# Kernel optimization log

Measured on AMD Instinct MI355X. Metric: run time of the kernel, lower is better.

The kernel has to match this reference:

```python
import jax, jax.numpy as jnp
import numpy as np

B, T, C, HS = 16, 2048, 2048, 256  # batch, seq (=BLOCK_SIZE), N_EMBD, head_size


def setup_inputs() -> dict:
    key = jax.random.key(0)
    k0, k1, k2, k3 = jax.random.split(key, 4)
    token_embd = jax.random.normal(k0, (B, T, C), dtype=jnp.float32)
    # nn.Linear(C, HS, bias=False); store as [C, HS] so projection is x @ W
    scale = 1.0 / np.sqrt(C)
    Wk = jax.random.normal(k1, (C, HS), dtype=jnp.float32) * scale
    Wq = jax.random.normal(k2, (C, HS), dtype=jnp.float32) * scale
    Wv = jax.random.normal(k3, (C, HS), dtype=jnp.float32) * scale
    return {"token_embd": token_embd, "Wk": Wk, "Wq": Wq, "Wv": Wv}


def reference(token_embd, Wk, Wq, Wv):
    Bc, Tc, Cc = token_embd.shape
    k = token_embd @ Wk  # [B,T,HS]
    q = token_embd @ Wq  # [B,T,HS]
    v = token_embd @ Wv  # [B,T,HS]
    # NOTE faithful quirks of the source: k @ q^T (not q @ k^T) and
    # MULTIPLY by sqrt(C) where C = N_EMBD.
    weights = jnp.einsum("bih,bjh->bij", k, q) * (Cc ** 0.5)  # [B,T,T]
    # causal mask: tril==0 (upper triangle, j>i) -> -inf
    i = jnp.arange(Tc)[:, None]
    j = jnp.arange(Tc)[None, :]
    weights = jnp.where(j > i, -jnp.inf, weights)
    # softmax over dim=1 (rows / first T axis), as in the source
    weights = jax.nn.softmax(weights, axis=1)
    # dropout p=0.0 / eval mode -> identity
    output = jnp.einsum("bij,bjh->bih", weights, v)  # [B,T,HS]
    return output
```

## Files before the change

kernel.cpp:

```cpp
#include <hip/hip_runtime.h>
#include <math.h>

#define Bn 16
#define Tn 2048
#define Cn 2048
#define HSn 256
#define SCALE 45.254833995939045f
#define NEG_BIG (-1e30f)
#define NT 16
#define NPAIR 136
#define WN 524288

typedef __attribute__((ext_vector_type(8))) short bf16x8;
typedef __attribute__((ext_vector_type(4))) float f32x4;
typedef unsigned short u16;
typedef unsigned int u32;

__device__ __forceinline__ u16 bf16_rn(float f) {
    u32 u = __float_as_uint(f);
    u += 0x7fffu + ((u >> 16) & 1u);
    return (u16)(u >> 16);
}
__device__ __forceinline__ float bf16_rn_f(float f) {
    return __uint_as_float((u32)bf16_rn(f) << 16);
}

#define GLOAD_LDS16(gp, lp)                                                      \
    __builtin_amdgcn_global_load_lds(                                            \
        (const __attribute__((address_space(1))) unsigned int*)(gp),             \
        (__attribute__((address_space(3))) unsigned int*)(lp), 16, 0, 0)

__global__ __launch_bounds__(256) void split_w_kernel(
    const float* __restrict__ Wk, const float* __restrict__ Wq,
    const float* __restrict__ Wv, u16* __restrict__ Wt)
{
    const int n = threadIdx.x, k = blockIdx.x, mat = blockIdx.y;
    const float* src = (mat == 0) ? Wk : (mat == 1) ? Wq : Wv;
    const float f = src[(long)k * HSn + n];
    const u32 u = __float_as_uint(f);
    const u16 hb = (u16)(u >> 16);
    const float fh = __uint_as_float(u & 0xffff0000u);
    const u16 lb = bf16_rn(f - fh);
    u16* base = Wt + (long)mat * 2 * WN;
    base[(long)n * Cn + k] = hb;
    base[WN + (long)n * Cn + k] = lb;
}

__global__ __launch_bounds__(256, 2) void projm_fused_kernel(
    const float* __restrict__ X, const u16* __restrict__ Wt,
    u16* __restrict__ Khi, u16* __restrict__ Klo,
    u16* __restrict__ Qhi, u16* __restrict__ Qlo, u16* __restrict__ Vbf)
{
    __shared__ u16 Ahi[2048], Alo[2048];
    __shared__ u16 Bbuf[20480];

    const int tid = threadIdx.x, l = tid & 63, w = tid >> 6;
    const int wm = w & 1, wn = w >> 1;
    const int m0 = blockIdx.x * 64, n0 = blockIdx.y * 128;

    int xoff[2], aoff[2];
    #pragma unroll
    for (int p = 0; p < 2; ++p) {
        const int idx4 = p * 256 + tid;
        const int row  = idx4 >> 3;
        const int kk4  = (idx4 & 7) * 4;
        xoff[p] = (m0 + row) * Cn + kk4;
        aoff[p] = (row >> 4) * 512 + (((row & 15) | ((kk4 >> 3) << 4)) * 8) + (kk4 & 7);
    }

    int wgoff[10];
    const int lbase = w * 10 * 512;
    #pragma unroll
    for (int j = 0; j < 10; ++j) {
        const int g    = w * 10 + j;
        const int half = g >> 3;
        const int cc   = g & 7;
        const int nrow = n0 + cc * 16 + (l & 15);
        wgoff[j] = half * WN + nrow * Cn + ((l >> 4) << 3);
    }

    f32x4 accK[2][4], accQ[2][4], accV[2][4];
    #pragma unroll
    for (int mt = 0; mt < 2; ++mt)
        #pragma unroll
        for (int nt = 0; nt < 4; ++nt)
            #pragma unroll
            for (int r = 0; r < 4; ++r) {
                accK[mt][nt][r] = 0.f; accQ[mt][nt][r] = 0.f; accV[mt][nt][r] = 0.f;
            }

    #pragma unroll 1
    for (int k0 = 0; k0 < Cn; k0 += 32) {
        const float4 xv0 = *(const float4*)(X + xoff[0] + k0);
        const float4 xv1 = *(const float4*)(X + xoff[1] + k0);
        #pragma unroll
        for (int j = 0; j < 10; ++j)
            GLOAD_LDS16(Wt + wgoff[j] + k0, Bbuf + lbase + j * 512);

        #pragma unroll
        for (int p = 0; p < 2; ++p) {
            const float4 xv = p ? xv1 : xv0;
            const float xf[4] = {xv.x, xv.y, xv.z, xv.w};
            ushort4 h4, l4;
            #pragma unroll
            for (int c = 0; c < 4; ++c) {
                const u32 u = __float_as_uint(xf[c]);
                ((u16*)&h4)[c] = (u16)(u >> 16);
                const float fh = __uint_as_float(u & 0xffff0000u);
                ((u16*)&l4)[c] = bf16_rn(xf[c] - fh);
            }
            *(ushort4*)(Ahi + aoff[p]) = h4;
            *(ushort4*)(Alo + aoff[p]) = l4;
        }
        __syncthreads();

        bf16x8 ah[2], al[2];
        #pragma unroll
        for (int mt = 0; mt < 2; ++mt) {
            ah[mt] = *(const bf16x8*)(Ahi + (wm * 2 + mt) * 512 + l * 8);
            al[mt] = *(const bf16x8*)(Alo + (wm * 2 + mt) * 512 + l * 8);
        }
        {
            bf16x8 bh[4], bl[4];
            #pragma unroll
            for (int nt = 0; nt < 4; ++nt) {
                bh[nt] = *(const bf16x8*)(Bbuf + (0 * 8 + wn * 4 + nt) * 512 + l * 8);
                bl[nt] = *(const bf16x8*)(Bbuf + (1 * 8 + wn * 4 + nt) * 512 + l * 8);
            }
            #pragma unroll
            for (int mt = 0; mt < 2; ++mt)
                #pragma unroll
                for (int nt = 0; nt < 4; ++nt) {
                    accK[mt][nt] = __builtin_amdgcn_mfma_f32_16x16x32_bf16(ah[mt], bh[nt], accK[mt][nt], 0, 0, 0);
                    accK[mt][nt] = __builtin_amdgcn_mfma_f32_16x16x32_bf16(ah[mt], bl[nt], accK[mt][nt], 0, 0, 0);
                    accK[mt][nt] = __builtin_amdgcn_mfma_f32_16x16x32_bf16(al[mt], bh[nt], accK[mt][nt], 0, 0, 0);
                }
        }
        {
            bf16x8 bh[4], bl[4];
            #pragma unroll
            for (int nt = 0; nt < 4; ++nt) {
                bh[nt] = *(const bf16x8*)(Bbuf + (2 * 8 + wn * 4 + nt) * 512 + l * 8);
                bl[nt] = *(const bf16x8*)(Bbuf + (3 * 8 + wn * 4 + nt) * 512 + l * 8);
            }
            #pragma unroll
            for (int mt = 0; mt < 2; ++mt)
                #pragma unroll
                for (int nt = 0; nt < 4; ++nt) {
                    accQ[mt][nt] = __builtin_amdgcn_mfma_f32_16x16x32_bf16(ah[mt], bh[nt], accQ[mt][nt], 0, 0, 0);
                    accQ[mt][nt] = __builtin_amdgcn_mfma_f32_16x16x32_bf16(ah[mt], bl[nt], accQ[mt][nt], 0, 0, 0);
                    accQ[mt][nt] = __builtin_amdgcn_mfma_f32_16x16x32_bf16(al[mt], bh[nt], accQ[mt][nt], 0, 0, 0);
                }
        }
        {
            bf16x8 bh[4];
            #pragma unroll
            for (int nt = 0; nt < 4; ++nt)
                bh[nt] = *(const bf16x8*)(Bbuf + (4 * 8 + wn * 4 + nt) * 512 + l * 8);
            #pragma unroll
            for (int mt = 0; mt < 2; ++mt)
                #pragma unroll
                for (int nt = 0; nt < 4; ++nt)
                    accV[mt][nt] = __builtin_amdgcn_mfma_f32_16x16x32_bf16(ah[mt], bh[nt], accV[mt][nt], 0, 0, 0);
        }
        __syncthreads();
    }

    const int quad = (l >> 4) * 4, col = l & 15;
    #pragma unroll
    for (int mt = 0; mt < 2; ++mt)
        #pragma unroll
        for (int nt = 0; nt < 4; ++nt)
            #pragma unroll
            for (int r = 0; r < 4; ++r) {
                const long i = m0 + wm * 32 + mt * 16 + quad + r;
                const int  j = n0 + wn * 64 + nt * 16 + col;
                {
                    const float f = accK[mt][nt][r];
                    const u32 u = __float_as_uint(f);
                    const u16 hb = (u16)(u >> 16);
                    const float fh = __uint_as_float(u & 0xffff0000u);
                    Khi[i * HSn + j] = hb;
                    Klo[i * HSn + j] = bf16_rn(f - fh);
                }
                {
                    const float f = accQ[mt][nt][r];
                    const u32 u = __float_as_uint(f);
                    const u16 hb = (u16)(u >> 16);
                    const float fh = __uint_as_float(u & 0xffff0000u);
                    Qhi[i * HSn + j] = hb;
                    Qlo[i * HSn + j] = bf16_rn(f - fh);
                }
                Vbf[i * HSn + j] = bf16_rn(accV[mt][nt][r]);
            }
}

__device__ __forceinline__ void score_tile_mfma(
    const u16* __restrict__ Khi, const u16* __restrict__ Klo,
    const u16* __restrict__ Qhi, const u16* __restrict__ Qlo,
    long base, int i0, int j0,
    u16* Abuf, u16* Bbuf, f32x4 (&acc)[4][4], int tid)
{
    const int l = tid & 63, w = tid >> 6;
    const int wm = w & 1, wn = w >> 1;
    const int lrow = l & 15, lk8 = (l >> 4) << 3;

    #pragma unroll
    for (int a = 0; a < 4; ++a)
        #pragma unroll
        for (int bb = 0; bb < 4; ++bb)
            #pragma unroll
            for (int r = 0; r < 4; ++r) acc[a][bb][r] = 0.f;

    for (int ks = 0; ks < 8; ++ks) {
        const int h0 = ks * 32;
        #pragma unroll
        for (int q = 0; q < 8; ++q) {
            const int c    = (w << 3) | q;
            const int side = c >> 4;
            const int cc   = c & 15;
            const int half = cc & 1;
            const int mt   = cc >> 1;
            const u16* src = side ? (half ? Qlo : Qhi) : (half ? Klo : Khi);
            const int row  = (side ? j0 : i0) + mt * 16 + lrow;
            const uint4 v  = *(const uint4*)(src + base + (long)row * HSn + h0 + lk8);
            u16* dst = (side ? Bbuf : Abuf) + cc * 512 + l * 8;
            *(uint4*)dst = v;
        }
        __syncthreads();
        bf16x8 bh[4], bl[4];
        #pragma unroll
        for (int nt = 0; nt < 4; ++nt) {
            const int c2 = (wn * 4 + nt) * 2;
            bh[nt] = *(const bf16x8*)(Bbuf + (c2    ) * 512 + l * 8);
            bl[nt] = *(const bf16x8*)(Bbuf + (c2 + 1) * 512 + l * 8);
        }
        #pragma unroll
        for (int mt = 0; mt < 4; ++mt) {
            const int c2 = (wm * 4 + mt) * 2;
            const bf16x8 ah = *(const bf16x8*)(Abuf + (c2    ) * 512 + l * 8);
            const bf16x8 al = *(const bf16x8*)(Abuf + (c2 + 1) * 512 + l * 8);
            #pragma unroll
            for (int nt = 0; nt < 4; ++nt) {
                acc[mt][nt] = __builtin_amdgcn_mfma_f32_16x16x32_bf16(ah, bh[nt], acc[mt][nt], 0, 0, 0);
                acc[mt][nt] = __builtin_amdgcn_mfma_f32_16x16x32_bf16(ah, bl[nt], acc[mt][nt], 0, 0, 0);
                acc[mt][nt] = __builtin_amdgcn_mfma_f32_16x16x32_bf16(al, bh[nt], acc[mt][nt], 0, 0, 0);
            }
        }
        __syncthreads();
    }
}

__device__ __forceinline__ void pair_from_p(int p, int& it, int& jt) {
    it = (int)((sqrtf(8.f * (float)p + 1.f) - 1.f) * 0.5f);
    while ((it + 1) * (it + 2) / 2 <= p) ++it;
    while (it * (it + 1) / 2 > p) --it;
    jt = p - it * (it + 1) / 2;
}

__global__ __launch_bounds__(256) void stats1_kernel(
    const u16* __restrict__ Khi, const u16* __restrict__ Klo,
    const u16* __restrict__ Qhi, const u16* __restrict__ Qlo,
    u16* __restrict__ Pm, u16* __restrict__ Pd)
{
    __shared__ u16 Abuf[8192], Bbuf[8192];
    __shared__ float redm[2][128], redd[2][128];

    const int tid = threadIdx.x, l = tid & 63, w = tid >> 6;
    const int wm = w & 1, wn = w >> 1;
    const int b = blockIdx.y;
    int it, jt; pair_from_p(blockIdx.x, it, jt);
    const long base = (long)b * Tn * HSn;

    f32x4 acc[4][4];
    score_tile_mfma(Khi, Klo, Qhi, Qlo, base, it * 128, jt * 128, Abuf, Bbuf, acc, tid);

    const int rquad = (l >> 4) * 4, col = l & 15;
    #pragma unroll
    for (int nt = 0; nt < 4; ++nt) {
        const int j = jt * 128 + wn * 64 + nt * 16 + col;
        float m = NEG_BIG;
        #pragma unroll
        for (int mt = 0; mt < 4; ++mt)
            #pragma unroll
            for (int r = 0; r < 4; ++r) {
                const int i = it * 128 + wm * 64 + mt * 16 + rquad + r;
                const float sv = (i >= j) ? acc[mt][nt][r] * SCALE : NEG_BIG;
                acc[mt][nt][r] = sv;
                m = fmaxf(m, sv);
            }
        m = fmaxf(m, __shfl_xor(m, 16));
        m = fmaxf(m, __shfl_xor(m, 32));
        float d = 0.f;
        #pragma unroll
        for (int mt = 0; mt < 4; ++mt)
            #pragma unroll
            for (int r = 0; r < 4; ++r)
                d += __expf(acc[mt][nt][r] - m);
        d += __shfl_xor(d, 16);
        d += __shfl_xor(d, 32);
        if (l < 16) {
            redm[wm][wn * 64 + nt * 16 + l] = m;
            redd[wm][wn * 64 + nt * 16 + l] = d;
        }
    }
    __syncthreads();
    if (tid < 128) {
        const float m0 = redm[0][tid], m1 = redm[1][tid];
        const float d0 = redd[0][tid], d1 = redd[1][tid];
        const float M = fmaxf(m0, m1);
        float D = d0 * __expf(m0 - M) + d1 * __expf(m1 - M);
        const float Mb = bf16_rn_f(M);
        D *= __expf(M - Mb);
        const long idx = ((long)b * NPAIR + blockIdx.x) * 128 + tid;
        Pm[idx] = (u16)(__float_as_uint(Mb) >> 16);
        Pd[idx] = bf16_rn(D);
    }
}

__global__ __launch_bounds__(128) void stats2_kernel(
    const u16* __restrict__ Pm, const u16* __restrict__ Pd,
    float* __restrict__ Ms, float* __restrict__ Rd)
{
    const int b = blockIdx.y, jt = blockIdx.x, jl = threadIdx.x;
    float M = NEG_BIG, D = 0.f;
    for (int it = jt; it < NT; ++it) {
        const int p = it * (it + 1) / 2 + jt;
        const long idx = ((long)b * NPAIR + p) * 128 + jl;
        const float m = __uint_as_float((u32)Pm[idx] << 16);
        const float d = __uint_as_float((u32)Pd[idx] << 16);
        const float Mn = fmaxf(M, m);
        D = D * __expf(M - Mn) + d * __expf(m - Mn);
        M = Mn;
    }
    Ms[(long)b * Tn + jt * 128 + jl] = M;
    Rd[(long)b * Tn + jt * 128 + jl] = 1.f / D;
}

__global__ __launch_bounds__(256) void out_kernel(
    const u16* __restrict__ Khi, const u16* __restrict__ Klo,
    const u16* __restrict__ Qhi, const u16* __restrict__ Qlo,
    const u16* __restrict__ Vbf, const float* __restrict__ Ms,
    const float* __restrict__ Rd, float* __restrict__ Out)
{
    __shared__ u16 u_lds[34816];
    u16* Abuf = u_lds;
    u16* Bbuf = u_lds + 8192;
    u16* Pf   = u_lds;
    u16* Vt   = u_lds + 17408;

    const int tid = threadIdx.x, l = tid & 63, w = tid >> 6;
    const int wm = w & 1, wn = w >> 1;
    const int b = blockIdx.y;
    int it, jt; pair_from_p(blockIdx.x, it, jt);
    const long base = (long)b * Tn * HSn;

    f32x4 acc[4][4];
    score_tile_mfma(Khi, Klo, Qhi, Qlo, base, it * 128, jt * 128, Abuf, Bbuf, acc, tid);

    const int rquad = (l >> 4) * 4, col = l & 15;
    float mj[4], rj[4];
    #pragma unroll
    for (int nt = 0; nt < 4; ++nt) {
        const int j = jt * 128 + wn * 64 + nt * 16 + col;
        mj[nt] = Ms[(long)b * Tn + j];
        rj[nt] = Rd[(long)b * Tn + j];
    }
    #pragma unroll
    for (int nt = 0; nt < 4; ++nt) {
        const int j = jt * 128 + wn * 64 + nt * 16 + col;
        #pragma unroll
        for (int mt = 0; mt < 4; ++mt)
            #pragma unroll
            for (int r = 0; r < 4; ++r) {
                const int i = it * 128 + wm * 64 + mt * 16 + rquad + r;
                const float pv = (i >= j)
                    ? __expf(acc[mt][nt][r] * SCALE - mj[nt]) * rj[nt] : 0.f;
                Pf[(wm * 64 + mt * 16 + rquad + r) * 136 + wn * 64 + nt * 16 + col]
                    = bf16_rn(pv);
            }
    }

    const int lrow = l & 15, lk8 = (l >> 4) << 3;
    for (int ph = 0; ph < 2; ++ph) {
        __syncthreads();
        {
            const int jj = tid & 127, hs = (tid >> 7) * 64;
            const long vbase = ((long)b * Tn + jt * 128 + jj) * HSn + ph * 128 + hs;
            #pragma unroll
            for (int qq = 0; qq < 8; ++qq) {
                union { uint4 v; u16 s[8]; } uu;
                uu.v = *(const uint4*)(Vbf + vbase + qq * 8);
                #pragma unroll
                for (int e = 0; e < 8; ++e)
                    Vt[(hs + qq * 8 + e) * 136 + jj] = uu.s[e];
            }
        }
        __syncthreads();

        f32x4 o[4][4];
        #pragma unroll
        for (int a = 0; a < 4; ++a)
            #pragma unroll
            for (int bb = 0; bb < 4; ++bb)
                #pragma unroll
                for (int r = 0; r < 4; ++r) o[a][bb][r] = 0.f;

        #pragma unroll
        for (int kj = 0; kj < 4; ++kj) {
            bf16x8 aP[4];
            #pragma unroll
            for (int mt = 0; mt < 4; ++mt)
                aP[mt] = *(const bf16x8*)(Pf + (wm * 64 + mt * 16 + lrow) * 136 + kj * 32 + lk8);
            #pragma unroll
            for (int nt = 0; nt < 4; ++nt) {
                const bf16x8 bV = *(const bf16x8*)(Vt + (wn * 64 + nt * 16 + lrow) * 136 + kj * 32 + lk8);
                #pragma unroll
                for (int mt = 0; mt < 4; ++mt)
                    o[mt][nt] = __builtin_amdgcn_mfma_f32_16x16x32_bf16(aP[mt], bV, o[mt][nt], 0, 0, 0);
            }
        }
        #pragma unroll
        for (int mt = 0; mt < 4; ++mt)
            #pragma unroll
            for (int nt = 0; nt < 4; ++nt)
                #pragma unroll
                for (int r = 0; r < 4; ++r) {
                    const int i = it * 128 + wm * 64 + mt * 16 + rquad + r;
                    const int h = ph * 128 + wn * 64 + nt * 16 + col;
                    atomicAdd(&Out[((long)b * Tn + i) * HSn + h], o[mt][nt][r]);
                }
    }
}

extern "C" void kernel_launch(void* const* d_in, const int* in_sizes, int n_in,
                              void* d_out, int out_size, void* d_ws, size_t ws_size,
                              hipStream_t stream) {
    const float* X  = (const float*)d_in[0];
    const float* Wk = (const float*)d_in[1];
    const float* Wq = (const float*)d_in[2];
    const float* Wv = (const float*)d_in[3];

    const long nE = (long)Bn * Tn * HSn;
    u16* Khi = (u16*)d_ws;
    u16* Klo = Khi + nE;
    u16* Qhi = Khi + 2 * nE;
    u16* Qlo = Khi + 3 * nE;
    u16* Vbf = Khi + 4 * nE;
    u16* Wt  = Khi + 5 * nE;
    u16* Pm  = Wt + 6L * WN;
    u16* Pd  = Pm + (long)Bn * NPAIR * 128;
    float* Ms = (float*)(Pd + (long)Bn * NPAIR * 128);
    float* Rd = Ms + (long)Bn * Tn;

    split_w_kernel<<<dim3(Cn, 3), 256, 0, stream>>>(Wk, Wq, Wv, Wt);
    projm_fused_kernel<<<dim3((Bn * Tn) / 64, HSn / 128), 256, 0, stream>>>(
        X, Wt, Khi, Klo, Qhi, Qlo, Vbf);
    stats1_kernel<<<dim3(NPAIR, Bn), 256, 0, stream>>>(Khi, Klo, Qhi, Qlo, Pm, Pd);
    stats2_kernel<<<dim3(NT, Bn), 128, 0, stream>>>(Pm, Pd, Ms, Rd);
    hipMemsetAsync(d_out, 0, (size_t)out_size * sizeof(float), stream);
    out_kernel<<<dim3(NPAIR, Bn), 256, 0, stream>>>(Khi, Klo, Qhi, Qlo, Vbf, Ms, Rd,
                                                    (float*)d_out);
}
```

Baseline: 1.094 ms.

## Software-pipeline projection and score loops, store V transposed for direct LDS loads

```diff
diff --git a/kernel.cpp b/kernel.cpp
--- a/kernel.cpp
+++ b/kernel.cpp
@@ -29,6 +29,11 @@
     __builtin_amdgcn_global_load_lds(                                            \
         (const __attribute__((address_space(1))) unsigned int*)(gp),             \
         (__attribute__((address_space(3))) unsigned int*)(lp), 16, 0, 0)
+
+#define WAITV0_LG0 asm volatile("s_waitcnt vmcnt(0) lgkmcnt(0)" ::: "memory")
+#define WAITV2_LG0 asm volatile("s_waitcnt vmcnt(2) lgkmcnt(0)" ::: "memory")
+#define WAITLG0    asm volatile("s_waitcnt lgkmcnt(0)" ::: "memory")
+#define BARRIER    __builtin_amdgcn_s_barrier()
 
 __global__ __launch_bounds__(256) void split_w_kernel(
     const float* __restrict__ Wk, const float* __restrict__ Wq,
@@ -49,7 +54,7 @@
 __global__ __launch_bounds__(256, 2) void projm_fused_kernel(
     const float* __restrict__ X, const u16* __restrict__ Wt,
     u16* __restrict__ Khi, u16* __restrict__ Klo,
-    u16* __restrict__ Qhi, u16* __restrict__ Qlo, u16* __restrict__ Vbf)
+    u16* __restrict__ Qhi, u16* __restrict__ Qlo, u16* __restrict__ VbfT)
 {
     __shared__ u16 Ahi[2048], Alo[2048];
     __shared__ u16 Bbuf[20480];
@@ -89,18 +94,12 @@
                 accK[mt][nt][r] = 0.f; accQ[mt][nt][r] = 0.f; accV[mt][nt][r] = 0.f;
             }
 
-    #pragma unroll 1
-    for (int k0 = 0; k0 < Cn; k0 += 32) {
-        const float4 xv0 = *(const float4*)(X + xoff[0] + k0);
-        const float4 xv1 = *(const float4*)(X + xoff[1] + k0);
-        #pragma unroll
-        for (int j = 0; j < 10; ++j)
-            GLOAD_LDS16(Wt + wgoff[j] + k0, Bbuf + lbase + j * 512);
-
+    float4 xA[2], xB[2];
+
+    auto convert_write = [&](const float4 (&xr)[2]) {
         #pragma unroll
         for (int p = 0; p < 2; ++p) {
-            const float4 xv = p ? xv1 : xv0;
-            const float xf[4] = {xv.x, xv.y, xv.z, xv.w};
+            const float xf[4] = {xr[p].x, xr[p].y, xr[p].z, xr[p].w};
             ushort4 h4, l4;
             #pragma unroll
             for (int c = 0; c < 4; ++c) {
@@ -112,8 +111,9 @@
             *(ushort4*)(Ahi + aoff[p]) = h4;
             *(ushort4*)(Alo + aoff[p]) = l4;
         }
-        __syncthreads();
-
+    };
+
+    auto mfma_all = [&]() {
         bf16x8 ah[2], al[2];
         #pragma unroll
         for (int mt = 0; mt < 2; ++mt) {
@@ -163,10 +163,42 @@
                 for (int nt = 0; nt < 4; ++nt)
                     accV[mt][nt] = __builtin_amdgcn_mfma_f32_16x16x32_bf16(ah[mt], bh[nt], accV[mt][nt], 0, 0, 0);
         }
-        __syncthreads();
+    };
+
+    xA[0] = *(const float4*)(X + xoff[0]);
+    xA[1] = *(const float4*)(X + xoff[1]);
+
+    #pragma unroll 1
+    for (int k0 = 0; k0 < Cn; k0 += 64) {
+        #pragma unroll
+        for (int j = 0; j < 10; ++j)
+            GLOAD_LDS16(Wt + wgoff[j] + k0, Bbuf + lbase + j * 512);
+        __builtin_amdgcn_sched_barrier(0);
+        xB[0] = *(const float4*)(X + xoff[0] + k0 + 32);
+        xB[1] = *(const float4*)(X + xoff[1] + k0 + 32);
+        convert_write(xA);
+        WAITV2_LG0;
+        BARRIER;
+        mfma_all();
+        WAITLG0;
+        BARRIER;
+        #pragma unroll
+        for (int j = 0; j < 10; ++j)
+            GLOAD_LDS16(Wt + wgoff[j] + k0 + 32, Bbuf + lbase + j * 512);
+        __builtin_amdgcn_sched_barrier(0);
+        const int kn = (k0 + 64 < Cn) ? k0 + 64 : 0;
+        xA[0] = *(const float4*)(X + xoff[0] + kn);
+        xA[1] = *(const float4*)(X + xoff[1] + kn);
+        convert_write(xB);
+        WAITV2_LG0;
+        BARRIER;
+        mfma_all();
+        WAITLG0;
+        BARRIER;
     }
 
     const int quad = (l >> 4) * 4, col = l & 15;
+    u16* Vlds = Bbuf;
     #pragma unroll
     for (int mt = 0; mt < 2; ++mt)
         #pragma unroll
@@ -178,28 +210,42 @@
                 {
                     const float f = accK[mt][nt][r];
                     const u32 u = __float_as_uint(f);
-                    const u16 hb = (u16)(u >> 16);
+                    Khi[i * HSn + j] = (u16)(u >> 16);
                     const float fh = __uint_as_float(u & 0xffff0000u);
-                    Khi[i * HSn + j] = hb;
                     Klo[i * HSn + j] = bf16_rn(f - fh);
                 }
                 {
                     const float f = accQ[mt][nt][r];
                     const u32 u = __float_as_uint(f);
-                    const u16 hb = (u16)(u >> 16);
+                    Qhi[i * HSn + j] = (u16)(u >> 16);
                     const float fh = __uint_as_float(u & 0xffff0000u);
-                    Qhi[i * HSn + j] = hb;
                     Qlo[i * HSn + j] = bf16_rn(f - fh);
                 }
-                Vbf[i * HSn + j] = bf16_rn(accV[mt][nt][r]);
-            }
+                Vlds[(wm * 32 + mt * 16 + quad + r) * 128 + wn * 64 + nt * 16 + col]
+                    = bf16_rn(accV[mt][nt][r]);
+            }
+    __syncthreads();
+    {
+        const int bidx = m0 >> 11, jb = m0 & (Tn - 1);
+        #pragma unroll
+        for (int hh = 0; hh < 4; ++hh) {
+            const int hl = hh * 32 + (tid >> 3);
+            const int h  = n0 + hl;
+            const int jl = (tid & 7) * 8;
+            union { uint4 v; u16 s[8]; } pk;
+            #pragma unroll
+            for (int e = 0; e < 8; ++e) pk.s[e] = Vlds[(jl + e) * 128 + hl];
+            *(uint4*)(VbfT + ((long)bidx * HSn + h) * Tn + jb + jl) = pk.v;
+        }
+    }
 }
 
 __device__ __forceinline__ void score_tile_mfma(
     const u16* __restrict__ Khi, const u16* __restrict__ Klo,
     const u16* __restrict__ Qhi, const u16* __restrict__ Qlo,
     long base, int i0, int j0,
-    u16* Abuf, u16* Bbuf, f32x4 (&acc)[4][4], int tid)
+    u16* Ab0, u16* Bb0, u16* Ab1, u16* Bb1,
+    f32x4 (&acc)[4][4], int tid)
 {
     const int l = tid & 63, w = tid >> 6;
     const int wm = w & 1, wn = w >> 1;
@@ -212,34 +258,38 @@
             #pragma unroll
             for (int r = 0; r < 4; ++r) acc[a][bb][r] = 0.f;
 
-    for (int ks = 0; ks < 8; ++ks) {
-        const int h0 = ks * 32;
+    const u16* hiP = wn ? Qhi : Khi;
+    const u16* loP = wn ? Qlo : Klo;
+    const int  t0  = wn ? j0 : i0;
+    long rowoff[4];
+    #pragma unroll
+    for (int m2 = 0; m2 < 4; ++m2) {
+        const int mt = (w & 1) * 4 + m2;
+        rowoff[m2] = base + (long)(t0 + mt * 16 + lrow) * HSn + lk8;
+    }
+    u16* dst0 = (wn ? Bb0 : Ab0) + (w & 1) * 8 * 512;
+    u16* dst1 = (wn ? Bb1 : Ab1) + (w & 1) * 8 * 512;
+
+    auto stage = [&](int h0, u16* dw) {
         #pragma unroll
         for (int q = 0; q < 8; ++q) {
-            const int c    = (w << 3) | q;
-            const int side = c >> 4;
-            const int cc   = c & 15;
-            const int half = cc & 1;
-            const int mt   = cc >> 1;
-            const u16* src = side ? (half ? Qlo : Qhi) : (half ? Klo : Khi);
-            const int row  = (side ? j0 : i0) + mt * 16 + lrow;
-            const uint4 v  = *(const uint4*)(src + base + (long)row * HSn + h0 + lk8);
-            u16* dst = (side ? Bbuf : Abuf) + cc * 512 + l * 8;
-            *(uint4*)dst = v;
-        }
-        __syncthreads();
+            const u16* sp = (q & 1) ? loP : hiP;
+            GLOAD_LDS16(sp + rowoff[q >> 1] + h0, dw + q * 512);
+        }
+    };
+    auto step = [&](const u16* Ab, const u16* Bb) {
         bf16x8 bh[4], bl[4];
         #pragma unroll
         for (int nt = 0; nt < 4; ++nt) {
             const int c2 = (wn * 4 + nt) * 2;
-            bh[nt] = *(const bf16x8*)(Bbuf + (c2    ) * 512 + l * 8);
-            bl[nt] = *(const bf16x8*)(Bbuf + (c2 + 1) * 512 + l * 8);
+            bh[nt] = *(const bf16x8*)(Bb + (c2    ) * 512 + l * 8);
+            bl[nt] = *(const bf16x8*)(Bb + (c2 + 1) * 512 + l * 8);
         }
         #pragma unroll
         for (int mt = 0; mt < 4; ++mt) {
             const int c2 = (wm * 4 + mt) * 2;
-            const bf16x8 ah = *(const bf16x8*)(Abuf + (c2    ) * 512 + l * 8);
-            const bf16x8 al = *(const bf16x8*)(Abuf + (c2 + 1) * 512 + l * 8);
+            const bf16x8 ah = *(const bf16x8*)(Ab + (c2    ) * 512 + l * 8);
+            const bf16x8 al = *(const bf16x8*)(Ab + (c2 + 1) * 512 + l * 8);
             #pragma unroll
             for (int nt = 0; nt < 4; ++nt) {
                 acc[mt][nt] = __builtin_amdgcn_mfma_f32_16x16x32_bf16(ah, bh[nt], acc[mt][nt], 0, 0, 0);
@@ -247,7 +297,21 @@
                 acc[mt][nt] = __builtin_amdgcn_mfma_f32_16x16x32_bf16(al, bh[nt], acc[mt][nt], 0, 0, 0);
             }
         }
-        __syncthreads();
+    };
+
+    stage(0, dst0);
+    WAITV0_LG0;
+    BARRIER;
+    #pragma unroll 1
+    for (int ks = 0; ks < 8; ks += 2) {
+        stage((ks + 1) * 32, dst1);
+        step(Ab0, Bb0);
+        WAITV0_LG0;
+        BARRIER;
+        if (ks + 2 < 8) stage((ks + 2) * 32, dst0);
+        step(Ab1, Bb1);
+        WAITV0_LG0;
+        BARRIER;
     }
 }
 
@@ -263,7 +327,7 @@
     const u16* __restrict__ Qhi, const u16* __restrict__ Qlo,
     u16* __restrict__ Pm, u16* __restrict__ Pd)
 {
-    __shared__ u16 Abuf[8192], Bbuf[8192];
+    __shared__ u16 s_lds[32768];
     __shared__ float redm[2][128], redd[2][128];
 
     const int tid = threadIdx.x, l = tid & 63, w = tid >> 6;
@@ -273,7 +337,8 @@
     const long base = (long)b * Tn * HSn;
 
     f32x4 acc[4][4];
-    score_tile_mfma(Khi, Klo, Qhi, Qlo, base, it * 128, jt * 128, Abuf, Bbuf, acc, tid);
+    score_tile_mfma(Khi, Klo, Qhi, Qlo, base, it * 128, jt * 128,
+                    s_lds, s_lds + 8192, s_lds + 16384, s_lds + 24576, acc, tid);
 
     const int rquad = (l >> 4) * 4, col = l & 15;
     #pragma unroll
@@ -340,23 +405,34 @@
 __global__ __launch_bounds__(256) void out_kernel(
     const u16* __restrict__ Khi, const u16* __restrict__ Klo,
     const u16* __restrict__ Qhi, const u16* __restrict__ Qlo,
-    const u16* __restrict__ Vbf, const float* __restrict__ Ms,
+    const u16* __restrict__ VbfT, const float* __restrict__ Ms,
     const float* __restrict__ Rd, float* __restrict__ Out)
 {
-    __shared__ u16 u_lds[34816];
-    u16* Abuf = u_lds;
-    u16* Bbuf = u_lds + 8192;
-    u16* Pf   = u_lds;
-    u16* Vt   = u_lds + 17408;
+    __shared__ u16 u_lds[33792];
+    u16* Pf    = u_lds;
+    u16* Vfrag = u_lds + 17408;
 
     const int tid = threadIdx.x, l = tid & 63, w = tid >> 6;
     const int wm = w & 1, wn = w >> 1;
+    const int lrow = l & 15, lk8 = (l >> 4) << 3;
     const int b = blockIdx.y;
     int it, jt; pair_from_p(blockIdx.x, it, jt);
     const long base = (long)b * Tn * HSn;
 
     f32x4 acc[4][4];
-    score_tile_mfma(Khi, Klo, Qhi, Qlo, base, it * 128, jt * 128, Abuf, Bbuf, acc, tid);
+    score_tile_mfma(Khi, Klo, Qhi, Qlo, base, it * 128, jt * 128,
+                    u_lds, u_lds + 8192, u_lds + 16384, u_lds + 24576, acc, tid);
+
+    auto stage_v = [&](int ph) {
+        #pragma unroll
+        for (int q = 0; q < 8; ++q) {
+            const int hh = ph * 128 + q * 16 + lrow;
+            const long ga = ((long)b * HSn + hh) * Tn + jt * 128 + w * 32 + lk8;
+            GLOAD_LDS16(VbfT + ga, Vfrag + (w * 8 + q) * 512);
+        }
+    };
+
+    stage_v(0);
 
     const int rquad = (l >> 4) * 4, col = l & 15;
     float mj[4], rj[4];
@@ -381,23 +457,7 @@
             }
     }
 
-    const int lrow = l & 15, lk8 = (l >> 4) << 3;
-    for (int ph = 0; ph < 2; ++ph) {
-        __syncthreads();
-        {
-            const int jj = tid & 127, hs = (tid >> 7) * 64;
-            const long vbase = ((long)b * Tn + jt * 128 + jj) * HSn + ph * 128 + hs;
-            #pragma unroll
-            for (int qq = 0; qq < 8; ++qq) {
-                union { uint4 v; u16 s[8]; } uu;
-                uu.v = *(const uint4*)(Vbf + vbase + qq * 8);
-                #pragma unroll
-                for (int e = 0; e < 8; ++e)
-                    Vt[(hs + qq * 8 + e) * 136 + jj] = uu.s[e];
-            }
-        }
-        __syncthreads();
-
+    auto pv_store = [&](int ph) {
         f32x4 o[4][4];
         #pragma unroll
         for (int a = 0; a < 4; ++a)
@@ -405,7 +465,6 @@
             for (int bb = 0; bb < 4; ++bb)
                 #pragma unroll
                 for (int r = 0; r < 4; ++r) o[a][bb][r] = 0.f;
-
         #pragma unroll
         for (int kj = 0; kj < 4; ++kj) {
             bf16x8 aP[4];
@@ -414,7 +473,7 @@
                 aP[mt] = *(const bf16x8*)(Pf + (wm * 64 + mt * 16 + lrow) * 136 + kj * 32 + lk8);
             #pragma unroll
             for (int nt = 0; nt < 4; ++nt) {
-                const bf16x8 bV = *(const bf16x8*)(Vt + (wn * 64 + nt * 16 + lrow) * 136 + kj * 32 + lk8);
+                const bf16x8 bV = *(const bf16x8*)(Vfrag + (kj * 8 + wn * 4 + nt) * 512 + l * 8);
                 #pragma unroll
                 for (int mt = 0; mt < 4; ++mt)
                     o[mt][nt] = __builtin_amdgcn_mfma_f32_16x16x32_bf16(aP[mt], bV, o[mt][nt], 0, 0, 0);
@@ -430,7 +489,14 @@
                     const int h = ph * 128 + wn * 64 + nt * 16 + col;
                     atomicAdd(&Out[((long)b * Tn + i) * HSn + h], o[mt][nt][r]);
                 }
-    }
+    };
+
+    __syncthreads();
+    pv_store(0);
+    __syncthreads();
+    stage_v(1);
+    __syncthreads();
+    pv_store(1);
 }
 
 extern "C" void kernel_launch(void* const* d_in, const int* in_sizes, int n_in,
@@ -446,7 +512,7 @@
     u16* Klo = Khi + nE;
     u16* Qhi = Khi + 2 * nE;
     u16* Qlo = Khi + 3 * nE;
-    u16* Vbf = Khi + 4 * nE;
+    u16* VbfT = Khi + 4 * nE;
     u16* Wt  = Khi + 5 * nE;
     u16* Pm  = Wt + 6L * WN;
     u16* Pd  = Pm + (long)Bn * NPAIR * 128;
@@ -455,10 +521,10 @@
 
     split_w_kernel<<<dim3(Cn, 3), 256, 0, stream>>>(Wk, Wq, Wv, Wt);
     projm_fused_kernel<<<dim3((Bn * Tn) / 64, HSn / 128), 256, 0, stream>>>(
-        X, Wt, Khi, Klo, Qhi, Qlo, Vbf);
+        X, Wt, Khi, Klo, Qhi, Qlo, VbfT);
     stats1_kernel<<<dim3(NPAIR, Bn), 256, 0, stream>>>(Khi, Klo, Qhi, Qlo, Pm, Pd);
     stats2_kernel<<<dim3(NT, Bn), 128, 0, stream>>>(Pm, Pd, Ms, Rd);
     hipMemsetAsync(d_out, 0, (size_t)out_size * sizeof(float), stream);
-    out_kernel<<<dim3(NPAIR, Bn), 256, 0, stream>>>(Khi, Klo, Qhi, Qlo, Vbf, Ms, Rd,
+    out_kernel<<<dim3(NPAIR, Bn), 256, 0, stream>>>(Khi, Klo, Qhi, Qlo, VbfT, Ms, Rd,
                                                     (float*)d_out);
 }
```

Result: faster. 1.066 ms (-2.5%).
